# Performance work log

Hardware: AMD Instinct MI355X
Metric: run time of the kernel (lower is better)

Reference implementation:

```python
import jax, jax.numpy as jnp
import numpy as np

N, M, D = 100000, 50000, 256


def setup_inputs() -> dict:
    key = jax.random.key(0)
    k1, k2, k3 = jax.random.split(key, 3)
    self_tensor = jax.random.normal(k1, (N, D), dtype=jnp.float32)
    updates = jax.random.normal(k2, (M, D), dtype=jnp.float32)
    index = jax.random.randint(k3, (M, D), 0, N, dtype=jnp.int32)
    return {"self_tensor": self_tensor, "index": index, "updates": updates, "axis": 0}


def reference(self_tensor, index, updates, axis):
    # torch.scatter_add(out, 0, index, updates):
    #   out[index[i, j], j] += updates[i, j]
    assert axis == 0, "reference implements scatter along axis 0"
    m, d = index.shape
    cols = jnp.broadcast_to(jnp.arange(d, dtype=index.dtype)[None, :], (m, d))
    return self_tensor.at[index, cols].add(updates)
```

## Files before the change

kernel.cpp:

```cpp
#include <hip/hip_runtime.h>

#define DCOLS 256
#define RB 128
#define NBINP 1024
#define MAT_OFF 16384
#define MAT_CAP (4u<<20)
#define PAIRS_OFF (MAT_OFF + MAT_CAP)
#define BLK4 1024
#define SUBS 4
#define CHUNK4 (BLK4 * SUBS)

typedef unsigned int u32;
typedef unsigned short u16;
typedef unsigned long long u64;

__global__ void copy_f4(const float4* __restrict__ src, float4* __restrict__ dst, int n4) {
    int i = blockIdx.x * blockDim.x + threadIdx.x;
    int stride = gridDim.x * blockDim.x;
    for (; i < n4; i += stride) dst[i] = src[i];
}

__global__ void scatter_add4(const int4* __restrict__ index,
                             const float4* __restrict__ upd,
                             float* __restrict__ out, int n4) {
    int i = blockIdx.x * blockDim.x + threadIdx.x;
    int stride = gridDim.x * blockDim.x;
    for (; i < n4; i += stride) {
        int4 idx  = index[i];
        float4 u  = upd[i];
        int j = (i << 2) & (DCOLS - 1);
        atomicAdd(&out[idx.x * DCOLS + j + 0], u.x);
        atomicAdd(&out[idx.y * DCOLS + j + 1], u.y);
        atomicAdd(&out[idx.z * DCOLS + j + 2], u.z);
        atomicAdd(&out[idx.w * DCOLS + j + 3], u.w);
    }
}

__global__ void __launch_bounds__(256) hist_blocks(const int4* __restrict__ idx4,
                                                   u32* __restrict__ mat, int n4) {
    __shared__ u32 hist[NBINP];
    int t = threadIdx.x;
    int b0 = blockIdx.x * CHUNK4;
    for (int i = t; i < NBINP; i += 256) hist[i] = 0;
    __syncthreads();
#pragma unroll
    for (int k = 0; k < 16; ++k) {
        int p = b0 + t + 256 * k;
        if (p < n4) {
            int4 v = idx4[p];
            atomicAdd(&hist[((u32)v.x) >> 7], 1u);
            atomicAdd(&hist[((u32)v.y) >> 7], 1u);
            atomicAdd(&hist[((u32)v.z) >> 7], 1u);
            atomicAdd(&hist[((u32)v.w) >> 7], 1u);
        }
    }
    __syncthreads();
    u32 base = (u32)blockIdx.x * NBINP;
    for (int i = t; i < NBINP; i += 256) mat[base + i] = hist[i];
}

__global__ void __launch_bounds__(64) scan_blocks(u32* __restrict__ mat,
                                                  u32* __restrict__ total, int nblk) {
    int bin = blockIdx.x;
    int lane = threadIdx.x;
    u32 carry = 0;
    int rounds = (nblk + 63) / 64;
    for (int r = 0; r < rounds; ++r) {
        int blk = r * 64 + lane;
        u32 v = (blk < nblk) ? mat[(u32)blk * NBINP + bin] : 0u;
        u32 incl = v;
#pragma unroll
        for (int d = 1; d < 64; d <<= 1) {
            u32 y = __shfl_up(incl, (unsigned)d, 64);
            if (lane >= d) incl += y;
        }
        if (blk < nblk) mat[(u32)blk * NBINP + bin] = carry + incl - v;
        carry += (u32)__shfl(incl, 63, 64);
    }
    if (lane == 0) total[bin] = carry;
}

__global__ void scan_binbases(const u32* __restrict__ total, u32* __restrict__ start) {
    __shared__ u32 tmp[1024];
    int t = threadIdx.x;
    u32 v = total[t];
    tmp[t] = v;
    __syncthreads();
    for (int off = 1; off < 1024; off <<= 1) {
        u32 a = (t >= off) ? tmp[t - off] : 0u;
        __syncthreads();
        tmp[t] += a;
        __syncthreads();
    }
    start[t] = tmp[t] - v;
}

__global__ void __launch_bounds__(256, 3) scatter_det(const int4* __restrict__ idx4,
                                                      const float4* __restrict__ upd4,
                                                      const u32* __restrict__ mat,
                                                      const u32* __restrict__ start,
                                                      u64* __restrict__ pairs, int n4) {
    __shared__ u32 hist[NBINP];
    __shared__ u32 basep[NBINP];
    __shared__ u16 excl16[NBINP];
    __shared__ u32 wtot[4];
    __shared__ u64 stage[4096];

    int t = threadIdx.x;
    int lane = t & 63, wid = t >> 6;
    int b0 = blockIdx.x * CHUNK4;
    u32 mbase = (u32)blockIdx.x * NBINP;

    for (int i = t; i < NBINP; i += 256) basep[i] = start[i] + mat[mbase + i];

    for (int s = 0; s < SUBS; ++s) {
        int sbase = b0 + s * BLK4;
        int4 iv[4]; float4 uv[4];
#pragma unroll
        for (int k = 0; k < 4; ++k) {
            int p = sbase + t + 256 * k;
            if (p < n4) { iv[k] = idx4[p]; uv[k] = upd4[p]; }
        }
        for (int i = t; i < NBINP; i += 256) hist[i] = 0;
        __syncthreads();
#pragma unroll
        for (int k = 0; k < 4; ++k) {
            int p = sbase + t + 256 * k;
            if (p < n4) {
                atomicAdd(&hist[((u32)iv[k].x) >> 7], 1u);
                atomicAdd(&hist[((u32)iv[k].y) >> 7], 1u);
                atomicAdd(&hist[((u32)iv[k].z) >> 7], 1u);
                atomicAdd(&hist[((u32)iv[k].w) >> 7], 1u);
            }
        }
        __syncthreads();
        u32 c0 = hist[4 * t + 0], c1 = hist[4 * t + 1];
        u32 c2 = hist[4 * t + 2], c3 = hist[4 * t + 3];
        u32 tsum = c0 + c1 + c2 + c3;
        u32 incl = tsum;
#pragma unroll
        for (int d = 1; d < 64; d <<= 1) {
            u32 y = __shfl_up(incl, (unsigned)d, 64);
            if (lane >= d) incl += y;
        }
        if (lane == 63) wtot[wid] = incl;
        __syncthreads();
        u32 woff = 0;
#pragma unroll
        for (int w = 0; w < 4; ++w) woff += (w < wid) ? wtot[w] : 0u;
        u32 e0 = woff + incl - tsum;
        u32 e1 = e0 + c0, e2 = e1 + c1, e3 = e2 + c2;
        excl16[4 * t + 0] = (u16)e0; excl16[4 * t + 1] = (u16)e1;
        excl16[4 * t + 2] = (u16)e2; excl16[4 * t + 3] = (u16)e3;
        hist[4 * t + 0] = e0; hist[4 * t + 1] = e1;
        hist[4 * t + 2] = e2; hist[4 * t + 3] = e3;
        __syncthreads();
        u32 colbase = (4u * (u32)t) & 255u;
#pragma unroll
        for (int k = 0; k < 4; ++k) {
            int p = sbase + t + 256 * k;
            if (p >= n4) continue;
            int rows[4] = {iv[k].x, iv[k].y, iv[k].z, iv[k].w};
            float vals[4] = {uv[k].x, uv[k].y, uv[k].z, uv[k].w};
#pragma unroll
            for (int c = 0; c < 4; ++c) {
                u32 row = (u32)rows[c];
                u32 slot = atomicAdd(&hist[row >> 7], 1u);
                stage[slot] = ((u64)__float_as_uint(vals[c]) << 32)
                            | ((u64)row << 8) | (u64)(colbase + (u32)c);
            }
        }
        __syncthreads();
        int sv = n4 - sbase; if (sv > BLK4) sv = BLK4; if (sv < 0) sv = 0;
        int scount = 4 * sv;
        for (int i = t; i < scount; i += 256) {
            u64 pr = stage[i];
            u32 rc  = (u32)pr & 0x1ffffffu;
            u32 row = rc >> 8;
            u32 bin = row >> 7;
            u32 d = basep[bin] + ((u32)i - (u32)excl16[bin]);
            u32 key = ((row & 127u) << 8) | (rc & 255u);
            pairs[d] = (pr & 0xffffffff00000000ull) | (u64)key;
        }
        __syncthreads();
        for (int b = t; b < NBINP; b += 256) basep[b] += hist[b] - (u32)excl16[b];
        __syncthreads();
    }
}

#define APPLY_P(p) { u32 k_ = (u32)(p); \
    if (((k_ >> 7) & 1u) == half) \
        atomicAdd(&acc[((k_ >> 8) & 127u) * 128u + (k_ & 127u)], \
                  __uint_as_float((u32)((p) >> 32))); }

__global__ void __launch_bounds__(1024, 8) apply_half(const float4* __restrict__ self4,
                                                      const u64* __restrict__ pairs,
                                                      const u32* __restrict__ start,
                                                      const u32* __restrict__ total,
                                                      float4* __restrict__ out4, int nrows) {
    __shared__ float acc[RB * 128];
    int t = threadIdx.x;
    int bin = blockIdx.x >> 1;
    u32 half = blockIdx.x & 1u;
    float4* acc4 = (float4*)acc;
    for (int i = t; i < RB * 32; i += 1024) acc4[i] = make_float4(0.f, 0.f, 0.f, 0.f);
    __syncthreads();

    u32 s = start[bin], e = s + total[bin];
    u32 i = s + (u32)t;
    for (; i + 3072u < e; i += 4096u) {
        u64 p0 = pairs[i];
        u64 p1 = pairs[i + 1024u];
        u64 p2 = pairs[i + 2048u];
        u64 p3 = pairs[i + 3072u];
        APPLY_P(p0); APPLY_P(p1); APPLY_P(p2); APPLY_P(p3);
    }
    for (; i < e; i += 1024u) { u64 p0 = pairs[i]; APPLY_P(p0); }
    __syncthreads();

    int r0 = bin * RB;
    int nr = nrows - r0; if (nr > RB) nr = RB;
    int tot4 = nr * 32;
    for (int i2 = t; i2 < tot4; i2 += 1024) {
        int r = i2 >> 5, c4 = i2 & 31;
        long g = (long)(r0 + r) * 64 + (long)(half * 32u) + c4;
        float4 a = self4[g];
        float4 c = acc4[(r << 5) + c4];
        a.x += c.x; a.y += c.y; a.z += c.z; a.w += c.w;
        out4[g] = a;
    }
}

extern "C" void kernel_launch(void* const* d_in, const int* in_sizes, int n_in,
                              void* d_out, int out_size, void* d_ws, size_t ws_size,
                              hipStream_t stream) {
    const float* self_t = (const float*)d_in[0];
    const int*   index  = (const int*)d_in[1];
    const float* upd    = (const float*)d_in[2];
    float* out = (float*)d_out;

    const int nd = out_size;
    const int md = in_sizes[1];
    const int nrows = nd / DCOLS;
    const int nbins = (nrows + RB - 1) / RB;
    int n4 = md / 4;
    int nblk = (n4 + CHUNK4 - 1) / CHUNK4;

    u32* total = (u32*)d_ws;
    u32* start = total + 1024;
    u32* mat   = (u32*)((char*)d_ws + MAT_OFF);
    u64* pairs = (u64*)((char*)d_ws + PAIRS_OFF);

    size_t need = (size_t)PAIRS_OFF + (size_t)md * 8;
    bool shape_ok = (nbins <= NBINP) && (nblk <= 1024) && !(md & 3) && !(nd & 3) &&
                    (md % DCOLS == 0) && (nd % DCOLS == 0);

    if (shape_ok && ws_size >= need) {
        hist_blocks<<<nblk, 256, 0, stream>>>((const int4*)index, mat, n4);
        scan_blocks<<<NBINP, 64, 0, stream>>>(mat, total, nblk);
        scan_binbases<<<1, 1024, 0, stream>>>(total, start);
        scatter_det<<<nblk, 256, 0, stream>>>((const int4*)index, (const float4*)upd,
                                              mat, start, pairs, n4);
        apply_half<<<2 * nbins, 1024, 0, stream>>>((const float4*)self_t, pairs, start,
                                                   total, (float4*)out, nrows);
    } else {
        copy_f4<<<2048, 256, 0, stream>>>((const float4*)self_t, (float4*)out, nd / 4);
        scatter_add4<<<4096, 256, 0, stream>>>((const int4*)index, (const float4*)upd, out, md / 4);
    }
}
```

Before: 204.1 us.

## Bin scatter pairs by row block and column half to avoid filtered reads

Doubles the bin count so each bin holds one 128-row block and one 128-column half. The apply kernel then reads only its own pairs instead of reading every pair twice and discarding half. The block histogram matrix is stored as u16 to shrink it, a strided hmap layout reorganises the shared-memory scan, and the next sub-chunk's inputs are prefetched into registers. In exchange the code uses more registers and shared memory in the scatter kernel, and the u16 counts rely on per-block bin counts staying under 65536.

New measurement: 239.4 us. +17.3%, slower.

```diff
diff --git a/kernel.cpp b/kernel.cpp
--- a/kernel.cpp
+++ b/kernel.cpp
@@ -2,7 +2,7 @@
 
 #define DCOLS 256
 #define RB 128
-#define NBINP 1024
+#define NBINP 2048
 #define MAT_OFF 16384
 #define MAT_CAP (4u<<20)
 #define PAIRS_OFF (MAT_OFF + MAT_CAP)
@@ -13,6 +13,8 @@
 typedef unsigned int u32;
 typedef unsigned short u16;
 typedef unsigned long long u64;
+
+__device__ __forceinline__ u32 hmap(u32 bin) { return ((bin & 7u) << 8) | (bin >> 3); }
 
 __global__ void copy_f4(const float4* __restrict__ src, float4* __restrict__ dst, int n4) {
     int i = blockIdx.x * blockDim.x + threadIdx.x;
@@ -37,10 +39,11 @@
 }
 
 __global__ void __launch_bounds__(256) hist_blocks(const int4* __restrict__ idx4,
-                                                   u32* __restrict__ mat, int n4) {
+                                                   u16* __restrict__ mat, int n4) {
     __shared__ u32 hist[NBINP];
     int t = threadIdx.x;
     int b0 = blockIdx.x * CHUNK4;
+    u32 hb = (u32)((t >> 5) & 1);
     for (int i = t; i < NBINP; i += 256) hist[i] = 0;
     __syncthreads();
 #pragma unroll
@@ -48,18 +51,18 @@
         int p = b0 + t + 256 * k;
         if (p < n4) {
             int4 v = idx4[p];
-            atomicAdd(&hist[((u32)v.x) >> 7], 1u);
-            atomicAdd(&hist[((u32)v.y) >> 7], 1u);
-            atomicAdd(&hist[((u32)v.z) >> 7], 1u);
-            atomicAdd(&hist[((u32)v.w) >> 7], 1u);
+            atomicAdd(&hist[(((u32)v.x) >> 7) * 2 + hb], 1u);
+            atomicAdd(&hist[(((u32)v.y) >> 7) * 2 + hb], 1u);
+            atomicAdd(&hist[(((u32)v.z) >> 7) * 2 + hb], 1u);
+            atomicAdd(&hist[(((u32)v.w) >> 7) * 2 + hb], 1u);
         }
     }
     __syncthreads();
     u32 base = (u32)blockIdx.x * NBINP;
-    for (int i = t; i < NBINP; i += 256) mat[base + i] = hist[i];
-}
-
-__global__ void __launch_bounds__(64) scan_blocks(u32* __restrict__ mat,
+    for (int i = t; i < NBINP; i += 256) mat[base + i] = (u16)hist[i];
+}
+
+__global__ void __launch_bounds__(64) scan_blocks(u16* __restrict__ mat,
                                                   u32* __restrict__ total, int nblk) {
     int bin = blockIdx.x;
     int lane = threadIdx.x;
@@ -67,14 +70,14 @@
     int rounds = (nblk + 63) / 64;
     for (int r = 0; r < rounds; ++r) {
         int blk = r * 64 + lane;
-        u32 v = (blk < nblk) ? mat[(u32)blk * NBINP + bin] : 0u;
+        u32 v = (blk < nblk) ? (u32)mat[(u32)blk * NBINP + bin] : 0u;
         u32 incl = v;
 #pragma unroll
         for (int d = 1; d < 64; d <<= 1) {
             u32 y = __shfl_up(incl, (unsigned)d, 64);
             if (lane >= d) incl += y;
         }
-        if (blk < nblk) mat[(u32)blk * NBINP + bin] = carry + incl - v;
+        if (blk < nblk) mat[(u32)blk * NBINP + bin] = (u16)(carry + incl - v);
         carry += (u32)__shfl(incl, 63, 64);
     }
     if (lane == 0) total[bin] = carry;
@@ -83,23 +86,26 @@
 __global__ void scan_binbases(const u32* __restrict__ total, u32* __restrict__ start) {
     __shared__ u32 tmp[1024];
     int t = threadIdx.x;
-    u32 v = total[t];
-    tmp[t] = v;
+    u32 a = total[2 * t], b = total[2 * t + 1];
+    u32 p = a + b;
+    tmp[t] = p;
     __syncthreads();
     for (int off = 1; off < 1024; off <<= 1) {
-        u32 a = (t >= off) ? tmp[t - off] : 0u;
-        __syncthreads();
-        tmp[t] += a;
-        __syncthreads();
-    }
-    start[t] = tmp[t] - v;
-}
-
-__global__ void __launch_bounds__(256, 3) scatter_det(const int4* __restrict__ idx4,
-                                                      const float4* __restrict__ upd4,
-                                                      const u32* __restrict__ mat,
-                                                      const u32* __restrict__ start,
-                                                      u64* __restrict__ pairs, int n4) {
+        u32 x = (t >= off) ? tmp[t - off] : 0u;
+        __syncthreads();
+        tmp[t] += x;
+        __syncthreads();
+    }
+    u32 e = tmp[t] - p;
+    start[2 * t] = e;
+    start[2 * t + 1] = e + a;
+}
+
+__global__ void __launch_bounds__(256, 3) scatter_det2(const int4* __restrict__ idx4,
+                                                       const float4* __restrict__ upd4,
+                                                       const u16* __restrict__ mat,
+                                                       const u32* __restrict__ start,
+                                                       u64* __restrict__ pairs, int n4) {
     __shared__ u32 hist[NBINP];
     __shared__ u32 basep[NBINP];
     __shared__ u16 excl16[NBINP];
@@ -110,33 +116,42 @@
     int lane = t & 63, wid = t >> 6;
     int b0 = blockIdx.x * CHUNK4;
     u32 mbase = (u32)blockIdx.x * NBINP;
-
-    for (int i = t; i < NBINP; i += 256) basep[i] = start[i] + mat[mbase + i];
+    u32 hb = (u32)((t >> 5) & 1);
+
+    for (int i = t; i < NBINP; i += 256) basep[i] = start[i] + (u32)mat[mbase + i];
+
+    int4 iv[4]; float4 uv[4]; int4 ivn[4]; float4 uvn[4];
+#pragma unroll
+    for (int k = 0; k < 4; ++k) {
+        int p = b0 + t + 256 * k;
+        if (p < n4) { iv[k] = idx4[p]; uv[k] = upd4[p]; }
+    }
 
     for (int s = 0; s < SUBS; ++s) {
         int sbase = b0 + s * BLK4;
-        int4 iv[4]; float4 uv[4];
-#pragma unroll
-        for (int k = 0; k < 4; ++k) {
-            int p = sbase + t + 256 * k;
-            if (p < n4) { iv[k] = idx4[p]; uv[k] = upd4[p]; }
-        }
         for (int i = t; i < NBINP; i += 256) hist[i] = 0;
         __syncthreads();
 #pragma unroll
         for (int k = 0; k < 4; ++k) {
             int p = sbase + t + 256 * k;
             if (p < n4) {
-                atomicAdd(&hist[((u32)iv[k].x) >> 7], 1u);
-                atomicAdd(&hist[((u32)iv[k].y) >> 7], 1u);
-                atomicAdd(&hist[((u32)iv[k].z) >> 7], 1u);
-                atomicAdd(&hist[((u32)iv[k].w) >> 7], 1u);
+                atomicAdd(&hist[hmap((((u32)iv[k].x) >> 7) * 2 + hb)], 1u);
+                atomicAdd(&hist[hmap((((u32)iv[k].y) >> 7) * 2 + hb)], 1u);
+                atomicAdd(&hist[hmap((((u32)iv[k].z) >> 7) * 2 + hb)], 1u);
+                atomicAdd(&hist[hmap((((u32)iv[k].w) >> 7) * 2 + hb)], 1u);
             }
         }
         __syncthreads();
-        u32 c0 = hist[4 * t + 0], c1 = hist[4 * t + 1];
-        u32 c2 = hist[4 * t + 2], c3 = hist[4 * t + 3];
-        u32 tsum = c0 + c1 + c2 + c3;
+        if (s < SUBS - 1) {
+#pragma unroll
+            for (int k = 0; k < 4; ++k) {
+                int p = sbase + BLK4 + t + 256 * k;
+                if (p < n4) { ivn[k] = idx4[p]; uvn[k] = upd4[p]; }
+            }
+        }
+        u32 c[8], tsum = 0;
+#pragma unroll
+        for (int j = 0; j < 8; ++j) { c[j] = hist[(u32)(j << 8) | (u32)t]; tsum += c[j]; }
         u32 incl = tsum;
 #pragma unroll
         for (int d = 1; d < 64; d <<= 1) {
@@ -148,12 +163,14 @@
         u32 woff = 0;
 #pragma unroll
         for (int w = 0; w < 4; ++w) woff += (w < wid) ? wtot[w] : 0u;
-        u32 e0 = woff + incl - tsum;
-        u32 e1 = e0 + c0, e2 = e1 + c1, e3 = e2 + c2;
-        excl16[4 * t + 0] = (u16)e0; excl16[4 * t + 1] = (u16)e1;
-        excl16[4 * t + 2] = (u16)e2; excl16[4 * t + 3] = (u16)e3;
-        hist[4 * t + 0] = e0; hist[4 * t + 1] = e1;
-        hist[4 * t + 2] = e2; hist[4 * t + 3] = e3;
+        u32 e = woff + incl - tsum;
+#pragma unroll
+        for (int j = 0; j < 8; ++j) {
+            u32 bin = 8u * (u32)t + (u32)j;
+            excl16[bin] = (u16)e;
+            hist[(u32)(j << 8) | (u32)t] = e;
+            e += c[j];
+        }
         __syncthreads();
         u32 colbase = (4u * (u32)t) & 255u;
 #pragma unroll
@@ -163,11 +180,11 @@
             int rows[4] = {iv[k].x, iv[k].y, iv[k].z, iv[k].w};
             float vals[4] = {uv[k].x, uv[k].y, uv[k].z, uv[k].w};
 #pragma unroll
-            for (int c = 0; c < 4; ++c) {
-                u32 row = (u32)rows[c];
-                u32 slot = atomicAdd(&hist[row >> 7], 1u);
-                stage[slot] = ((u64)__float_as_uint(vals[c]) << 32)
-                            | ((u64)row << 8) | (u64)(colbase + (u32)c);
+            for (int cc = 0; cc < 4; ++cc) {
+                u32 row = (u32)rows[cc];
+                u32 slot = atomicAdd(&hist[hmap((row >> 7) * 2 + hb)], 1u);
+                stage[slot] = ((u64)__float_as_uint(vals[cc]) << 32)
+                            | ((u64)row << 8) | (u64)(colbase + (u32)cc);
             }
         }
         __syncthreads();
@@ -177,45 +194,51 @@
             u64 pr = stage[i];
             u32 rc  = (u32)pr & 0x1ffffffu;
             u32 row = rc >> 8;
-            u32 bin = row >> 7;
+            u32 col8 = rc & 255u;
+            u32 bin = (row >> 7) * 2 + ((col8 >> 7) & 1u);
             u32 d = basep[bin] + ((u32)i - (u32)excl16[bin]);
-            u32 key = ((row & 127u) << 8) | (rc & 255u);
+            u32 key = ((row & 127u) << 8) | col8;
             pairs[d] = (pr & 0xffffffff00000000ull) | (u64)key;
         }
         __syncthreads();
-        for (int b = t; b < NBINP; b += 256) basep[b] += hist[b] - (u32)excl16[b];
-        __syncthreads();
-    }
-}
-
-#define APPLY_P(p) { u32 k_ = (u32)(p); \
-    if (((k_ >> 7) & 1u) == half) \
-        atomicAdd(&acc[((k_ >> 8) & 127u) * 128u + (k_ & 127u)], \
-                  __uint_as_float((u32)((p) >> 32))); }
-
-__global__ void __launch_bounds__(1024, 8) apply_half(const float4* __restrict__ self4,
+        for (int b = t; b < NBINP; b += 256)
+            basep[b] += hist[hmap((u32)b)] - (u32)excl16[b];
+        if (s < SUBS - 1) {
+#pragma unroll
+            for (int k = 0; k < 4; ++k) { iv[k] = ivn[k]; uv[k] = uvn[k]; }
+        }
+        __syncthreads();
+    }
+}
+
+#define ACC_P(p) { u32 k_ = (u32)(p); \
+    atomicAdd(&acc[((k_ >> 8) & 127u) * 128u + (k_ & 127u)], \
+              __uint_as_float((u32)((p) >> 32))); }
+
+__global__ void __launch_bounds__(1024, 2) apply_full(const float4* __restrict__ self4,
                                                       const u64* __restrict__ pairs,
                                                       const u32* __restrict__ start,
                                                       const u32* __restrict__ total,
                                                       float4* __restrict__ out4, int nrows) {
     __shared__ float acc[RB * 128];
     int t = threadIdx.x;
-    int bin = blockIdx.x >> 1;
-    u32 half = blockIdx.x & 1u;
+    int sb = blockIdx.x;
+    int bin = sb >> 1;
+    u32 half = (u32)(sb & 1);
     float4* acc4 = (float4*)acc;
     for (int i = t; i < RB * 32; i += 1024) acc4[i] = make_float4(0.f, 0.f, 0.f, 0.f);
     __syncthreads();
 
-    u32 s = start[bin], e = s + total[bin];
+    u32 s = start[sb], e = s + total[sb];
     u32 i = s + (u32)t;
     for (; i + 3072u < e; i += 4096u) {
         u64 p0 = pairs[i];
         u64 p1 = pairs[i + 1024u];
         u64 p2 = pairs[i + 2048u];
         u64 p3 = pairs[i + 3072u];
-        APPLY_P(p0); APPLY_P(p1); APPLY_P(p2); APPLY_P(p3);
-    }
-    for (; i < e; i += 1024u) { u64 p0 = pairs[i]; APPLY_P(p0); }
+        ACC_P(p0); ACC_P(p1); ACC_P(p2); ACC_P(p3);
+    }
+    for (; i < e; i += 1024u) { u64 p0 = pairs[i]; ACC_P(p0); }
     __syncthreads();
 
     int r0 = bin * RB;
@@ -247,21 +270,21 @@
     int nblk = (n4 + CHUNK4 - 1) / CHUNK4;
 
     u32* total = (u32*)d_ws;
-    u32* start = total + 1024;
-    u32* mat   = (u32*)((char*)d_ws + MAT_OFF);
+    u32* start = total + 2048;
+    u16* mat   = (u16*)((char*)d_ws + MAT_OFF);
     u64* pairs = (u64*)((char*)d_ws + PAIRS_OFF);
 
     size_t need = (size_t)PAIRS_OFF + (size_t)md * 8;
-    bool shape_ok = (nbins <= NBINP) && (nblk <= 1024) && !(md & 3) && !(nd & 3) &&
+    bool shape_ok = (2 * nbins <= NBINP) && (nblk <= 1024) && !(md & 3) && !(nd & 3) &&
                     (md % DCOLS == 0) && (nd % DCOLS == 0);
 
     if (shape_ok && ws_size >= need) {
         hist_blocks<<<nblk, 256, 0, stream>>>((const int4*)index, mat, n4);
         scan_blocks<<<NBINP, 64, 0, stream>>>(mat, total, nblk);
         scan_binbases<<<1, 1024, 0, stream>>>(total, start);
-        scatter_det<<<nblk, 256, 0, stream>>>((const int4*)index, (const float4*)upd,
-                                              mat, start, pairs, n4);
-        apply_half<<<2 * nbins, 1024, 0, stream>>>((const float4*)self_t, pairs, start,
+        scatter_det2<<<nblk, 256, 0, stream>>>((const int4*)index, (const float4*)upd,
+                                               mat, start, pairs, n4);
+        apply_full<<<2 * nbins, 1024, 0, stream>>>((const float4*)self_t, pairs, start,
                                                    total, (float4*)out, nrows);
     } else {
         copy_f4<<<2048, 256, 0, stream>>>((const float4*)self_t, (float4*)out, nd / 4);
```

## Prefetch next sub-chunk and fold bin base offsets into single bias table

Applied to the files above, without the earlier changes.

The scatter kernel now issues the global loads for the next sub-chunk while the current one is being scanned and staged, which hides load latency behind compute. Per-bin base and exclusive offsets are merged into one precomputed bias array held in registers and shared memory. This removes the 16-bit exclusive table, one barrier and the basep update loop, so shared memory use drops and the launch-bounds occupancy hint rises from 3 to 4. In exchange the kernel uses more registers for the prefetch buffers, and the wave totals now sit in bias slots 1020-1023, so the fast path requires at most 1020 bins.

After: 199.9 us. -2.1%, faster.

```diff
diff --git a/kernel.cpp b/kernel.cpp
--- a/kernel.cpp
+++ b/kernel.cpp
@@ -11,7 +11,6 @@
 #define CHUNK4 (BLK4 * SUBS)
 
 typedef unsigned int u32;
-typedef unsigned short u16;
 typedef unsigned long long u64;
 
 __global__ void copy_f4(const float4* __restrict__ src, float4* __restrict__ dst, int n4) {
@@ -95,15 +94,13 @@
     start[t] = tmp[t] - v;
 }
 
-__global__ void __launch_bounds__(256, 3) scatter_det(const int4* __restrict__ idx4,
-                                                      const float4* __restrict__ upd4,
-                                                      const u32* __restrict__ mat,
-                                                      const u32* __restrict__ start,
-                                                      u64* __restrict__ pairs, int n4) {
+__global__ void __launch_bounds__(256, 4) scatter_det3(const int4* __restrict__ idx4,
+                                                       const float4* __restrict__ upd4,
+                                                       const u32* __restrict__ mat,
+                                                       const u32* __restrict__ start,
+                                                       u64* __restrict__ pairs, int n4) {
     __shared__ u32 hist[NBINP];
-    __shared__ u32 basep[NBINP];
-    __shared__ u16 excl16[NBINP];
-    __shared__ u32 wtot[4];
+    __shared__ u32 bias[NBINP];
     __shared__ u64 stage[4096];
 
     int t = threadIdx.x;
@@ -111,18 +108,21 @@
     int b0 = blockIdx.x * CHUNK4;
     u32 mbase = (u32)blockIdx.x * NBINP;
 
-    for (int i = t; i < NBINP; i += 256) basep[i] = start[i] + mat[mbase + i];
+    uint4 s4 = ((const uint4*)start)[t];
+    uint4 m4 = ((const uint4*)(mat + mbase))[t];
+    u32 bp[4] = { s4.x + m4.x, s4.y + m4.y, s4.z + m4.z, s4.w + m4.w };
+
+    int4 iv[4]; float4 uv[4]; int4 ivn[4]; float4 uvn[4];
+#pragma unroll
+    for (int k = 0; k < 4; ++k) {
+        int p = b0 + t + 256 * k;
+        if (p < n4) { iv[k] = idx4[p]; uv[k] = upd4[p]; }
+    }
+    for (int i = t; i < NBINP; i += 256) hist[i] = 0;
+    __syncthreads();
 
     for (int s = 0; s < SUBS; ++s) {
         int sbase = b0 + s * BLK4;
-        int4 iv[4]; float4 uv[4];
-#pragma unroll
-        for (int k = 0; k < 4; ++k) {
-            int p = sbase + t + 256 * k;
-            if (p < n4) { iv[k] = idx4[p]; uv[k] = upd4[p]; }
-        }
-        for (int i = t; i < NBINP; i += 256) hist[i] = 0;
-        __syncthreads();
 #pragma unroll
         for (int k = 0; k < 4; ++k) {
             int p = sbase + t + 256 * k;
@@ -134,6 +134,13 @@
             }
         }
         __syncthreads();
+        if (s < SUBS - 1) {
+#pragma unroll
+            for (int k = 0; k < 4; ++k) {
+                int p = sbase + BLK4 + t + 256 * k;
+                if (p < n4) { ivn[k] = idx4[p]; uvn[k] = upd4[p]; }
+            }
+        }
         u32 c0 = hist[4 * t + 0], c1 = hist[4 * t + 1];
         u32 c2 = hist[4 * t + 2], c3 = hist[4 * t + 3];
         u32 tsum = c0 + c1 + c2 + c3;
@@ -143,17 +150,23 @@
             u32 y = __shfl_up(incl, (unsigned)d, 64);
             if (lane >= d) incl += y;
         }
-        if (lane == 63) wtot[wid] = incl;
+        if (lane == 63) bias[1020 + wid] = incl;
         __syncthreads();
         u32 woff = 0;
 #pragma unroll
-        for (int w = 0; w < 4; ++w) woff += (w < wid) ? wtot[w] : 0u;
-        u32 e0 = woff + incl - tsum;
-        u32 e1 = e0 + c0, e2 = e1 + c1, e3 = e2 + c2;
-        excl16[4 * t + 0] = (u16)e0; excl16[4 * t + 1] = (u16)e1;
-        excl16[4 * t + 2] = (u16)e2; excl16[4 * t + 3] = (u16)e3;
-        hist[4 * t + 0] = e0; hist[4 * t + 1] = e1;
-        hist[4 * t + 2] = e2; hist[4 * t + 3] = e3;
+        for (int w = 0; w < 4; ++w) woff += (w < wid) ? bias[1020 + w] : 0u;
+        u32 e = woff + incl - tsum;
+        u32 cc[4] = {c0, c1, c2, c3};
+#pragma unroll
+        for (int j = 0; j < 4; ++j) {
+            u32 bin = 4u * (u32)t + (u32)j;
+            if (cc[j]) {
+                bias[bin] = bp[j] - e;
+                hist[bin] = e;
+                bp[j] += cc[j];
+            }
+            e += cc[j];
+        }
         __syncthreads();
         u32 colbase = (4u * (u32)t) & 255u;
 #pragma unroll
@@ -178,12 +191,15 @@
             u32 rc  = (u32)pr & 0x1ffffffu;
             u32 row = rc >> 8;
             u32 bin = row >> 7;
-            u32 d = basep[bin] + ((u32)i - (u32)excl16[bin]);
+            u32 d = bias[bin] + (u32)i;
             u32 key = ((row & 127u) << 8) | (rc & 255u);
             pairs[d] = (pr & 0xffffffff00000000ull) | (u64)key;
         }
-        __syncthreads();
-        for (int b = t; b < NBINP; b += 256) basep[b] += hist[b] - (u32)excl16[b];
+        for (int i = t; i < NBINP; i += 256) hist[i] = 0;
+        if (s < SUBS - 1) {
+#pragma unroll
+            for (int k = 0; k < 4; ++k) { iv[k] = ivn[k]; uv[k] = uvn[k]; }
+        }
         __syncthreads();
     }
 }
@@ -252,15 +268,15 @@
     u64* pairs = (u64*)((char*)d_ws + PAIRS_OFF);
 
     size_t need = (size_t)PAIRS_OFF + (size_t)md * 8;
-    bool shape_ok = (nbins <= NBINP) && (nblk <= 1024) && !(md & 3) && !(nd & 3) &&
+    bool shape_ok = (nbins <= 1020) && (nblk <= 1024) && !(md & 3) && !(nd & 3) &&
                     (md % DCOLS == 0) && (nd % DCOLS == 0);
 
     if (shape_ok && ws_size >= need) {
         hist_blocks<<<nblk, 256, 0, stream>>>((const int4*)index, mat, n4);
         scan_blocks<<<NBINP, 64, 0, stream>>>(mat, total, nblk);
         scan_binbases<<<1, 1024, 0, stream>>>(total, start);
-        scatter_det<<<nblk, 256, 0, stream>>>((const int4*)index, (const float4*)upd,
-                                              mat, start, pairs, n4);
+        scatter_det3<<<nblk, 256, 0, stream>>>((const int4*)index, (const float4*)upd,
+                                               mat, start, pairs, n4);
         apply_half<<<2 * nbins, 1024, 0, stream>>>((const float4*)self_t, pairs, start,
                                                    total, (float4*)out, nrows);
     } else {
```
